# Kernel optimization log

Measured on AMD Instinct MI355X. Metric: run time of the kernel, lower is better.

## Reference

```python
import jax, jax.numpy as jnp
import numpy as np

NEARZERO = 1e-05
NMUL = 1
UH_LEN = 15  # gamma unit-hydrograph kernel length (days)

PHY_BOUNDS = {
    'ddf_min': [0.0, 20.0], 'ddf_plus': [0.0, 20.0], 'Tbm': [-2.0, 3.0],
    'Kcum': [0.01, 0.2], 'fcmin': [0.0, 0.1], 'fcmin_plus': [0.01, 0.25],
    'Ccum': [0.005, 0.05], 'Tbf': [-5.0, 2.0], 'Kf': [0.0, 5.0],
    'exp_fe': [0.0, 1.0], 'ET_efficiency': [0.0, 3.0], 'coef_runoff': [0.0, 1.0],
    'coef_vadose2phreatic': [1e-05, 0.02], 'coef_vadose': [0.0, 0.1],
    'coef_phreatic': [1e-05, 0.01], 'vadose_max_level': [0.001, 500.0],
}
ROUT_BOUNDS = {'alpha1': [0.3, 20.0], 'beta1': [0.01, 5.0], 'alpha2': [0.5, 13.0], 'beta2': [0.15, 1.5]}


def change_param_range(p, b):
    return b[0] + p * (b[1] - b[0])


def gamma_uh(alpha, beta, L=UH_LEN):
    # Discretized gamma unit hydrograph, normalized. alpha, beta: [G]
    t = jnp.arange(L, dtype=jnp.float32) + 0.5  # [L]
    w = t ** (alpha[:, None] - 1.0) * jnp.exp(-t / beta[:, None])  # [G, L]
    return w / jnp.sum(w, axis=1, keepdims=True)


def uh_conv(q, uh):
    # Causal per-grid convolution. q: [T, G], uh: [G, L] -> [T, G]
    T, G = q.shape
    L = uh.shape[1]
    qpad = jnp.concatenate([jnp.zeros((L - 1, G), q.dtype), q], axis=0)
    # shifts[l] = q delayed by l steps
    shifts = jnp.stack([qpad[L - 1 - l:L - 1 - l + T] for l in range(L)], axis=0)  # [L, T, G]
    return jnp.einsum('ltg,gl->tg', shifts, uh)


def setup_inputs() -> dict:
    key = jax.random.key(0)
    k1, k2, k3, k4 = jax.random.split(key, 4)
    T, G = 1460, 5000
    prcp = jax.random.uniform(k1, (T, G), jnp.float32) * 20.0   # mm/day, >= 0
    tmean = jax.random.normal(k2, (T, G), jnp.float32) * 10.0   # deg C, crosses 0
    pet = jax.random.uniform(k3, (T, G), jnp.float32) * 5.0     # mm/day
    x_phy = jnp.stack([prcp, tmean, pet], axis=-1)              # [T, G, 3]
    parameters = jax.random.normal(k4, (T, G, 20), jnp.float32)
    return {'x_phy': x_phy, 'parameters': parameters}


def hmets_forward(x_phy, parameters):
    names = list(PHY_BOUNDS.keys())
    nphy = len(names)
    T, G, _ = x_phy.shape
    # unpack_parameters
    phy = jax.nn.sigmoid(parameters[:, :, :nphy * NMUL]).reshape(T, G, nphy, NMUL)
    rout = jax.nn.sigmoid(parameters[-1, :, nphy * NMUL:])  # [G, 4]
    # descale: dynamic_params is empty -> all params static from last step, [G, NMUL]
    pd = {n: change_param_range(phy[-1, :, i, :], PHY_BOUNDS[n]) for i, n in enumerate(names)}
    rd = {n: change_param_range(rout[:, i], ROUT_BOUNDS[n]) for i, n in enumerate(ROUT_BOUNDS)}
    Vmax = pd['vadose_max_level']

    full = lambda: jnp.full((G, NMUL), NEARZERO, jnp.float32)
    init = (full(), full(), full(), 0.5 * Vmax, full())  # SNOW, WATER_IN_SNOWPACK, CUMSNOWMELT, VADOSE, PHREATIC

    def step(carry, inp):
        S, W, C, V, P = carry
        Pp, Tt, PETt = inp
        Pp = Pp[:, None]; Tt = Tt[:, None]; PETt = PETt[:, None]  # [G, 1] broadcast to nmul
        rain = Pp * (Tt >= 0.0).astype(Pp.dtype)
        snow = Pp * (Tt < 0.0).astype(Pp.dtype)
        # overnight refreezing of liquid water in snowpack
        pot_fr = pd['Kf'] * jnp.maximum(pd['Tbf'] - Tt, NEARZERO) ** pd['exp_fe']
        fr = jnp.minimum(pot_fr, W)
        W = W - fr
        S = S + fr
        # degree-day snowmelt with cumulative-melt-dependent ddf
        ddf = jnp.minimum(pd['ddf_min'] + pd['ddf_plus'], pd['ddf_min'] * (1.0 + pd['Kcum'] * C))
        melt = jnp.minimum(jnp.maximum(ddf * (Tt - pd['Tbm']), 0.0), S + snow)
        S = S + snow - melt
        C = (C + melt) * (S > NEARZERO).astype(S.dtype)
        # snowpack water retention
        wrf = jnp.maximum((pd['fcmin'] + pd['fcmin_plus']) * (1.0 - pd['Ccum'] * C), pd['fcmin'])
        wr = wrf * S
        wtmp = W + melt + rain
        wa = jnp.maximum(wtmp - wr, 0.0)
        W = jnp.where(wa > 0.0, wr, wtmp)
        # evapotranspiration + runoff partitioning
        RET = pd['ET_efficiency'] * PETt
        ratio = V / Vmax
        ht0 = pd['coef_runoff'] * ratio * wa                       # surface runoff
        infil = jnp.maximum(wa - ht0 - RET, 0.0)
        ht1 = pd['coef_runoff'] * ratio * ratio * infil            # delayed runoff
        ht2 = pd['coef_vadose'] * V                                # interflow
        v2p = pd['coef_vadose2phreatic'] * V                       # percolation
        V = V + (infil - ht1) - ht2 - v2p
        over = jnp.maximum(V - Vmax, 0.0)                          # vadose overflow -> delayed runoff
        V = V - over
        ht1 = ht1 + over
        P = P + v2p
        ht3 = pd['coef_phreatic'] * P                              # baseflow
        P = P - ht3
        return (S, W, C, V, P), (ht0, ht1, ht2, ht3)

    forc = (x_phy[:, :, 0], x_phy[:, :, 1], x_phy[:, :, 2])
    _, (ht0, ht1, ht2, ht3) = jax.lax.scan(step, init, forc)  # each [T, G, NMUL]
    # average over nmul components (muwts=None -> uniform mean)
    q_surf = ht0.mean(axis=-1)
    q_del = ht1.mean(axis=-1)
    q_gw = (ht2 + ht3).mean(axis=-1)
    # gamma UH routing
    uh1 = gamma_uh(rd['alpha1'], rd['beta1'])
    uh2 = gamma_uh(rd['alpha2'], rd['beta2'])
    Q = uh_conv(q_surf, uh1) + uh_conv(q_del, uh2) + q_gw  # [T, G]
    return Q


def reference(x_phy, parameters):
    return hmets_forward(x_phy, parameters)
```

## Files before the change

### kernel.cpp

```cpp
#include <hip/hip_runtime.h>

#define T_STEPS 1460
#define G_CELLS 5000
#define NPARAM 20
#define UH_L 15
#define NZ 1e-5f
#define KT 16
#define DCH 10
#define NCH (T_STEPS / DCH)

__device__ __forceinline__ float sigmoidf(float x) {
    return 1.0f / (1.0f + __expf(-x));
}

__device__ __forceinline__ float fast_pow(float x, float y) {
    return __builtin_amdgcn_exp2f(y * __builtin_amdgcn_logf(x));
}

__global__ void uh_kernel(const float* __restrict__ params,
                          float* __restrict__ uh1T, float* __restrict__ uh2T) {
    int g = blockIdx.x * blockDim.x + threadIdx.x;
    if (g >= G_CELLS) return;
    const float* pr = params + ((size_t)(T_STEPS - 1) * G_CELLS + g) * NPARAM;
    float a1 = 0.3f  + sigmoidf(pr[16]) * (20.0f - 0.3f);
    float b1 = 0.01f + sigmoidf(pr[17]) * (5.0f  - 0.01f);
    float a2 = 0.5f  + sigmoidf(pr[18]) * (13.0f - 0.5f);
    float b2 = 0.15f + sigmoidf(pr[19]) * (1.5f  - 0.15f);
    float w1[UH_L], w2[UH_L];
    float s1 = 0.f, s2 = 0.f;
    #pragma unroll
    for (int l = 0; l < UH_L; ++l) {
        float t = (float)l + 0.5f;
        w1[l] = fast_pow(t, a1 - 1.0f) * __expf(-t / b1);
        w2[l] = fast_pow(t, a2 - 1.0f) * __expf(-t / b2);
        s1 += w1[l]; s2 += w2[l];
    }
    float r1 = 1.0f / s1, r2 = 1.0f / s2;
    #pragma unroll
    for (int l = 0; l < UH_L; ++l) {
        uh1T[l * G_CELLS + g] = w1[l] * r1;
        uh2T[l * G_CELLS + g] = w2[l] * r2;
    }
}

__global__ void __launch_bounds__(64, 1) rec_kernel(
        const float* __restrict__ x_phy, const float* __restrict__ params,
        float2* __restrict__ q2, float* __restrict__ qgw) {
    int g = blockIdx.x * 64 + threadIdx.x;
    if (g >= G_CELLS) return;

    const float* pr = params + ((size_t)(T_STEPS - 1) * G_CELLS + g) * NPARAM;
    float p[16];
    #pragma unroll
    for (int i = 0; i < 16; ++i) p[i] = sigmoidf(pr[i]);

    const float ddf_min    = p[0] * 20.f;
    const float ddf_plus   = p[1] * 20.f;
    const float Tbm        = -2.f + p[2] * 5.f;
    const float Kcum       = 0.01f + p[3] * 0.19f;
    const float fcmin      = p[4] * 0.1f;
    const float fcmin_plus = 0.01f + p[5] * 0.24f;
    const float Ccum       = 0.005f + p[6] * 0.045f;
    const float Tbf        = -5.f + p[7] * 7.f;
    const float Kf         = p[8] * 5.f;
    const float exp_fe     = p[9];
    const float ET_eff     = p[10] * 3.f;
    const float cr         = p[11];
    const float cvp        = 1e-5f + p[12] * (0.02f - 1e-5f);
    const float cv         = p[13] * 0.1f;
    const float cp         = 1e-5f + p[14] * (0.01f - 1e-5f);
    const float Vmax       = 0.001f + p[15] * (500.f - 0.001f);

    const float invVmax = 1.0f / Vmax;
    const float ddf_sum = ddf_min + ddf_plus;
    const float dmK     = ddf_min * Kcum;
    const float fc_sum  = fcmin + fcmin_plus;
    const float fcC     = fc_sum * Ccum;

    float S = NZ, W = NZ, C = NZ, V = 0.5f * Vmax, P = NZ;

    const int STR = G_CELLS * 3;
    const float* base = x_phy + (size_t)g * 3;

    float A[DCH][3], B[DCH][3];

    auto LOAD = [&](float (&buf)[DCH][3], int c) {
        const float* pp = base + (size_t)c * DCH * STR;
        #pragma unroll
        for (int j = 0; j < DCH; ++j) {
            buf[j][0] = pp[0]; buf[j][1] = pp[1]; buf[j][2] = pp[2];
            pp += STR;
        }
    };

    auto COMPUTE = [&](float (&buf)[DCH][3], int c) {
        float ob[DCH][3];
        #pragma unroll
        for (int j = 0; j < DCH; ++j) {
            float Pp = buf[j][0], Tt = buf[j][1], PE = buf[j][2];

            float rain = (Tt >= 0.f) ? Pp : 0.f;
            float snow = Pp - rain;
            float xb   = fmaxf(Tbf - Tt, NZ);
            float pot_fr = Kf * fast_pow(xb, exp_fe);
            float fr   = fminf(pot_fr, W);
            W -= fr; S += fr;
            float ddf  = fminf(ddf_sum, fmaf(dmK, C, ddf_min));
            float Ssn  = S + snow;
            float melt = fminf(fmaxf(ddf * (Tt - Tbm), 0.f), Ssn);
            S = Ssn - melt;
            C = (S > NZ) ? (C + melt) : 0.f;
            float wrf  = fmaxf(fmaf(-fcC, C, fc_sum), fcmin);
            float wr   = wrf * S;
            float wtmp = W + melt + rain;
            float wa   = fmaxf(wtmp - wr, 0.f);
            W = (wa > 0.f) ? wr : wtmp;
            float RET   = ET_eff * PE;
            float ratio = V * invVmax;
            float crr   = cr * ratio;
            float ht0   = crr * wa;
            float infil = fmaxf(wa - ht0 - RET, 0.f);
            float ht1   = crr * ratio * infil;
            float ht2   = cv * V;
            float v2p   = cvp * V;
            V = V + infil - ht1 - ht2 - v2p;
            float over  = fmaxf(V - Vmax, 0.f);
            V -= over; ht1 += over;
            P += v2p;
            float ht3 = cp * P;
            P -= ht3;

            ob[j][0] = ht0; ob[j][1] = ht1; ob[j][2] = ht2 + ht3;
        }
        size_t t0 = (size_t)c * DCH;
        #pragma unroll
        for (int j = 0; j < DCH; ++j) {
            q2 [(t0 + j) * G_CELLS + g] = make_float2(ob[j][0], ob[j][1]);
            qgw[(t0 + j) * G_CELLS + g] = ob[j][2];
        }
    };

    LOAD(A, 0);
    for (int c = 0; c < NCH; c += 2) {
        LOAD(B, c + 1);
        COMPUTE(A, c);
        if (c + 2 < NCH) LOAD(A, c + 2);
        COMPUTE(B, c + 1);
    }
}

__global__ void __launch_bounds__(256) fir_kernel(
        const float2* __restrict__ q2, const float* __restrict__ qgw,
        const float* __restrict__ uh1T, const float* __restrict__ uh2T,
        float* __restrict__ out) {
    int g = blockIdx.x * 256 + threadIdx.x;
    if (g >= G_CELLS) return;
    int t0 = blockIdx.y * KT;

    float w1[UH_L], w2[UH_L];
    #pragma unroll
    for (int l = 0; l < UH_L; ++l) {
        w1[l] = uh1T[l * G_CELLS + g];
        w2[l] = uh2T[l * G_CELLS + g];
    }
    float r0[UH_L], r1[UH_L];
    #pragma unroll
    for (int k = 0; k < UH_L - 1; ++k) {
        int tq = t0 - (UH_L - 1) + k;
        if (tq >= 0) {
            float2 v = q2[(size_t)tq * G_CELLS + g];
            r0[k] = v.x; r1[k] = v.y;
        } else { r0[k] = 0.f; r1[k] = 0.f; }
    }
    #pragma unroll
    for (int j = 0; j < KT; ++j) {
        int t = t0 + j;
        if (t < T_STEPS) {
            const int ns = (j + UH_L - 1) % UH_L;
            float2 v = q2[(size_t)t * G_CELLS + g];
            r0[ns] = v.x; r1[ns] = v.y;
            float acc = qgw[(size_t)t * G_CELLS + g];
            #pragma unroll
            for (int l = 0; l < UH_L; ++l) {
                const int idx = (j - l + UH_L - 1) % UH_L;
                acc += r0[idx] * w1[l] + r1[idx] * w2[l];
            }
            out[(size_t)t * G_CELLS + g] = acc;
        }
    }
}

extern "C" void kernel_launch(void* const* d_in, const int* in_sizes, int n_in,
                              void* d_out, int out_size, void* d_ws, size_t ws_size,
                              hipStream_t stream) {
    const float* x_phy  = (const float*)d_in[0];
    const float* params = (const float*)d_in[1];
    float* out = (float*)d_out;

    char* ws = (char*)d_ws;
    float2* q2   = (float2*)ws;
    float*  qgw  = (float*)(ws + (size_t)T_STEPS * G_CELLS * 8);
    float*  uh1T = (float*)(ws + (size_t)T_STEPS * G_CELLS * 12);
    float*  uh2T = uh1T + UH_L * G_CELLS;

    uh_kernel<<<(G_CELLS + 255) / 256, 256, 0, stream>>>(params, uh1T, uh2T);
    rec_kernel<<<(G_CELLS + 63) / 64, 64, 0, stream>>>(x_phy, params, q2, qgw);
    dim3 fgrid((G_CELLS + 255) / 256, (T_STEPS + KT - 1) / KT);
    fir_kernel<<<fgrid, 256, 0, stream>>>(q2, qgw, uh1T, uh2T, out);
}
```

Baseline: 929.8 us.

## Split recurrence into snow and soil wavefronts pipelined through shared memory

```diff
diff --git a/kernel.cpp b/kernel.cpp
--- a/kernel.cpp
+++ b/kernel.cpp
@@ -5,7 +5,7 @@
 #define NPARAM 20
 #define UH_L 15
 #define NZ 1e-5f
-#define KT 16
+#define KT 32
 #define DCH 10
 #define NCH (T_STEPS / DCH)
 
@@ -43,62 +43,66 @@
     }
 }
 
-__global__ void __launch_bounds__(64, 1) rec_kernel(
+__global__ void __launch_bounds__(128, 1) rec_kernel(
         const float* __restrict__ x_phy, const float* __restrict__ params,
         float2* __restrict__ q2, float* __restrict__ qgw) {
-    int g = blockIdx.x * 64 + threadIdx.x;
-    if (g >= G_CELLS) return;
-
-    const float* pr = params + ((size_t)(T_STEPS - 1) * G_CELLS + g) * NPARAM;
-    float p[16];
-    #pragma unroll
-    for (int i = 0; i < 16; ++i) p[i] = sigmoidf(pr[i]);
-
-    const float ddf_min    = p[0] * 20.f;
-    const float ddf_plus   = p[1] * 20.f;
-    const float Tbm        = -2.f + p[2] * 5.f;
-    const float Kcum       = 0.01f + p[3] * 0.19f;
-    const float fcmin      = p[4] * 0.1f;
-    const float fcmin_plus = 0.01f + p[5] * 0.24f;
-    const float Ccum       = 0.005f + p[6] * 0.045f;
-    const float Tbf        = -5.f + p[7] * 7.f;
-    const float Kf         = p[8] * 5.f;
-    const float exp_fe     = p[9];
-    const float ET_eff     = p[10] * 3.f;
-    const float cr         = p[11];
-    const float cvp        = 1e-5f + p[12] * (0.02f - 1e-5f);
-    const float cv         = p[13] * 0.1f;
-    const float cp         = 1e-5f + p[14] * (0.01f - 1e-5f);
-    const float Vmax       = 0.001f + p[15] * (500.f - 0.001f);
-
-    const float invVmax = 1.0f / Vmax;
+    const int lane = threadIdx.x & 63;
+    const int wid  = threadIdx.x >> 6;
+    const int g    = blockIdx.x * 64 + lane;
+    const int gc   = (g < G_CELLS) ? g : (G_CELLS - 1);
+    const bool valid = (g < G_CELLS);
+
+    __shared__ float s_wa[2][DCH][64];
+
+    const float* pr = params + ((size_t)(T_STEPS - 1) * G_CELLS + gc) * NPARAM;
+    const int STR = G_CELLS * 3;
+
+    const float ddf_min    = sigmoidf(pr[0]) * 20.f;
+    const float ddf_plus   = sigmoidf(pr[1]) * 20.f;
+    const float Tbm        = -2.f + sigmoidf(pr[2]) * 5.f;
+    const float Kcum       = 0.01f + sigmoidf(pr[3]) * 0.19f;
+    const float fcmin      = sigmoidf(pr[4]) * 0.1f;
+    const float fcmin_plus = 0.01f + sigmoidf(pr[5]) * 0.24f;
+    const float Ccum       = 0.005f + sigmoidf(pr[6]) * 0.045f;
+    const float Tbf        = -5.f + sigmoidf(pr[7]) * 7.f;
+    const float Kf         = sigmoidf(pr[8]) * 5.f;
+    const float exp_fe     = sigmoidf(pr[9]);
     const float ddf_sum = ddf_min + ddf_plus;
     const float dmK     = ddf_min * Kcum;
     const float fc_sum  = fcmin + fcmin_plus;
     const float fcC     = fc_sum * Ccum;
-
-    float S = NZ, W = NZ, C = NZ, V = 0.5f * Vmax, P = NZ;
-
-    const int STR = G_CELLS * 3;
-    const float* base = x_phy + (size_t)g * 3;
-
-    float A[DCH][3], B[DCH][3];
-
-    auto LOAD = [&](float (&buf)[DCH][3], int c) {
+    float S = NZ, W = NZ, C = NZ;
+
+    const float ET_eff = sigmoidf(pr[10]) * 3.f;
+    const float cr     = sigmoidf(pr[11]);
+    const float cvp    = 1e-5f + sigmoidf(pr[12]) * (0.02f - 1e-5f);
+    const float cv     = sigmoidf(pr[13]) * 0.1f;
+    const float cp     = 1e-5f + sigmoidf(pr[14]) * (0.01f - 1e-5f);
+    const float Vmax   = 0.001f + sigmoidf(pr[15]) * (500.f - 0.001f);
+    const float invVmax = 1.0f / Vmax;
+    float V = 0.5f * Vmax, P = NZ;
+
+    const float* base  = x_phy + (size_t)gc * 3;
+    const float* baseE = x_phy + (size_t)gc * 3 + 2;
+
+    float A[DCH][2], B[DCH][2];
+    float PA[DCH], PB[DCH];
+
+    auto LOADPT = [&](float (&buf)[DCH][2], int c) {
         const float* pp = base + (size_t)c * DCH * STR;
         #pragma unroll
+        for (int j = 0; j < DCH; ++j) { buf[j][0] = pp[0]; buf[j][1] = pp[1]; pp += STR; }
+    };
+    auto LOADPE = [&](float (&buf)[DCH], int c) {
+        const float* pp = baseE + (size_t)c * DCH * STR;
+        #pragma unroll
+        for (int j = 0; j < DCH; ++j) { buf[j] = *pp; pp += STR; }
+    };
+
+    auto SNOW = [&](float (&buf)[DCH][2], int c) {
+        #pragma unroll
         for (int j = 0; j < DCH; ++j) {
-            buf[j][0] = pp[0]; buf[j][1] = pp[1]; buf[j][2] = pp[2];
-            pp += STR;
-        }
-    };
-
-    auto COMPUTE = [&](float (&buf)[DCH][3], int c) {
-        float ob[DCH][3];
-        #pragma unroll
-        for (int j = 0; j < DCH; ++j) {
-            float Pp = buf[j][0], Tt = buf[j][1], PE = buf[j][2];
-
+            float Pp = buf[j][0], Tt = buf[j][1];
             float rain = (Tt >= 0.f) ? Pp : 0.f;
             float snow = Pp - rain;
             float xb   = fmaxf(Tbf - Tt, NZ);
@@ -115,7 +119,16 @@
             float wtmp = W + melt + rain;
             float wa   = fmaxf(wtmp - wr, 0.f);
             W = (wa > 0.f) ? wr : wtmp;
-            float RET   = ET_eff * PE;
+            s_wa[c & 1][j][lane] = wa;
+        }
+    };
+
+    auto VP = [&](float (&pe)[DCH], int c) {
+        size_t t0 = (size_t)c * DCH;
+        #pragma unroll
+        for (int j = 0; j < DCH; ++j) {
+            float wa   = s_wa[c & 1][j][lane];
+            float RET  = ET_eff * pe[j];
             float ratio = V * invVmax;
             float crr   = cr * ratio;
             float ht0   = crr * wa;
@@ -129,23 +142,30 @@
             P += v2p;
             float ht3 = cp * P;
             P -= ht3;
-
-            ob[j][0] = ht0; ob[j][1] = ht1; ob[j][2] = ht2 + ht3;
-        }
-        size_t t0 = (size_t)c * DCH;
-        #pragma unroll
-        for (int j = 0; j < DCH; ++j) {
-            q2 [(t0 + j) * G_CELLS + g] = make_float2(ob[j][0], ob[j][1]);
-            qgw[(t0 + j) * G_CELLS + g] = ob[j][2];
-        }
-    };
-
-    LOAD(A, 0);
-    for (int c = 0; c < NCH; c += 2) {
-        LOAD(B, c + 1);
-        COMPUTE(A, c);
-        if (c + 2 < NCH) LOAD(A, c + 2);
-        COMPUTE(B, c + 1);
+            if (valid) {
+                q2 [(t0 + j) * G_CELLS + g] = make_float2(ht0, ht1);
+                qgw[(t0 + j) * G_CELLS + g] = ht2 + ht3;
+            }
+        }
+    };
+
+    if (wid == 0) {
+        LOADPT(A, 0); LOADPT(B, 1);
+        SNOW(A, 0);
+    } else {
+        LOADPE(PA, 0); LOADPE(PB, 1);
+    }
+    __syncthreads();
+
+    for (int c = 0; c < NCH; ++c) {
+        if (wid == 0) {
+            if (c + 2 < NCH) LOADPT((c & 1) ? B : A, c + 2);
+            if (c + 1 < NCH) SNOW(((c + 1) & 1) ? B : A, c + 1);
+        } else {
+            VP((c & 1) ? PB : PA, c);
+            if (c + 2 < NCH) LOADPE((c & 1) ? PB : PA, c + 2);
+        }
+        __syncthreads();
     }
 }
 
@@ -204,7 +224,7 @@
     float*  uh2T = uh1T + UH_L * G_CELLS;
 
     uh_kernel<<<(G_CELLS + 255) / 256, 256, 0, stream>>>(params, uh1T, uh2T);
-    rec_kernel<<<(G_CELLS + 63) / 64, 64, 0, stream>>>(x_phy, params, q2, qgw);
+    rec_kernel<<<(G_CELLS + 63) / 64, 128, 0, stream>>>(x_phy, params, q2, qgw);
     dim3 fgrid((G_CELLS + 255) / 256, (T_STEPS + KT - 1) / KT);
     fir_kernel<<<fgrid, 256, 0, stream>>>(q2, qgw, uh1T, uh2T, out);
 }
```

New measurement: 889.8 us. -4.3%, faster.
